# Performance work log

Hardware: AMD Instinct MI355X
Metric: run time of the kernel (lower is better)

The kernel has to match this reference:

```python
import jax, jax.numpy as jnp
import numpy as np

D_MODEL = 768
N_HEADS = 12
D_HEAD = 64
N_MEM = 3072
ALPHA = 0.1
EPS = 1e-5
W_SCALE = 0.02  # standard init scale so energies/grads stay well-conditioned


def setup_inputs() -> dict:
    key = jax.random.key(0)
    k0, k1, k2, k3 = jax.random.split(key, 4)
    B, S = 8, 1024
    x = jax.random.normal(k0, (B, S, D_MODEL), jnp.float32)
    gamma = jnp.ones((1,), jnp.float32)                      # scalar LN gamma (ET uses a single gamma)
    delta = jnp.zeros((D_MODEL,), jnp.float32)               # LN bias
    Wq = jax.random.normal(k1, (N_HEADS, D_HEAD, D_MODEL), jnp.float32) * W_SCALE
    Wk = jax.random.normal(k2, (N_HEADS, D_HEAD, D_MODEL), jnp.float32) * W_SCALE
    beta = jnp.ones((N_HEADS,), jnp.float32) / np.sqrt(D_HEAD)  # per-head beta init 1/sqrt(d_head)
    xi = jax.random.normal(k3, (N_MEM, D_MODEL), jnp.float32) * W_SCALE
    return {"x": x, "gamma": gamma, "delta": delta, "Wq": Wq, "Wk": Wk,
            "beta": beta, "xi": xi, "n_steps": 12}


def _total_energy(x, gamma, delta, Wq, Wk, beta, xi):
    # --- EnergyLayerNorm: g = dL/dx, E_ln = <x, g> - L ---
    mean = jnp.mean(x, axis=-1, keepdims=True)
    xm = x - mean
    var = jnp.mean(xm * xm, axis=-1, keepdims=True)
    std = jnp.sqrt(var + EPS)
    g = gamma * xm / std + delta                       # (B,S,D)
    L = jnp.sum(D_MODEL * gamma * std) + jnp.sum(delta * x)
    e_ln = jnp.sum(x * g) - L
    # --- EnergyAttention: E = -sum_{b,h,q} (1/beta_h) * logsumexp_k(beta_h * Q.K) ---
    q = jnp.einsum('bsd,hyd->bhsy', g, Wq)
    k = jnp.einsum('bsd,hyd->bhsy', g, Wk)
    A = jnp.einsum('bhqy,bhky->bhqk', q, k)            # (B,H,S,S)
    lse = jax.nn.logsumexp(beta[None, :, None, None] * A, axis=-1)  # (B,H,S)
    e_attn = -jnp.sum(lse / beta[None, :, None])
    # --- HopfieldNetwork: E = -1/2 sum relu(g @ xi^T)^2 ---
    h = jnp.einsum('bsd,md->bsm', g, xi)               # (B,S,M)
    e_hop = -0.5 * jnp.sum(jnp.square(jax.nn.relu(h)))
    return e_ln + e_attn + e_hop


def reference(x, gamma, delta, Wq, Wk, beta, xi, n_steps):
    grad_fn = jax.grad(_total_energy, argnums=0)

    def step(state, _):
        return state - ALPHA * grad_fn(state, gamma, delta, Wq, Wk, beta, xi), None

    final, _ = jax.lax.scan(step, x, None, length=n_steps)
    return final
```

## Files before the change

kernel.cpp:

```cpp
#include <hip/hip_runtime.h>
#include <hip/hip_bf16.h>
#include <stdint.h>

#define T_TOK 8192
#define DM    768
#define NH    12
#define DH    64
#define SEQ   1024
#define NBH   96
#define NMEM  3072
#define NUP   4608
#define ALPHA 0.1f
#define EPS   1e-5f
#define NSTEPS 12
#define PAD   72
#define SPLITK 4

typedef unsigned short us;
typedef __bf16 bf16x8 __attribute__((ext_vector_type(8)));
typedef float  f32x4  __attribute__((ext_vector_type(4)));

__device__ __forceinline__ us f2bf(float f) {
  uint32_t u = __builtin_bit_cast(uint32_t, f);
  u += 0x7fffu + ((u >> 16) & 1u);
  return (us)(u >> 16);
}

__device__ __forceinline__ f32x4 mfma16(bf16x8 a, bf16x8 b, f32x4 c) {
  return __builtin_amdgcn_mfma_f32_16x16x32_bf16(a, b, c, 0, 0, 0);
}

__device__ __forceinline__ void gld16(const void* g, void* l) {
  __builtin_amdgcn_global_load_lds(
      (const __attribute__((address_space(1))) void*)(uintptr_t)g,
      (__attribute__((address_space(3))) void*)(uint32_t)(uintptr_t)l,
      16, 0, 0);
}

__device__ __forceinline__ float block_sum(float v, float* sb, int tid) {
#pragma unroll
  for (int d = 32; d >= 1; d >>= 1) v += __shfl_xor(v, d);
  __syncthreads();
  if ((tid & 63) == 0) sb[tid >> 6] = v;
  __syncthreads();
  return sb[0] + sb[1] + sb[2] + sb[3];
}

__global__ __launch_bounds__(256) void pack_w(const float* __restrict__ Wq,
                                              const float* __restrict__ Wk,
                                              const float* __restrict__ xi,
                                              us* __restrict__ Wup, us* __restrict__ WdT) {
  int idx = blockIdx.x * 256 + threadIdx.x;
  if (idx >= NUP * DM) return;
  int r = idx / DM, d = idx - r * DM;
  float v = (r < 768) ? Wq[idx] : (r < 1536 ? Wk[idx - 768 * DM] : xi[idx - 1536 * DM]);
  us h = f2bf(v);
  Wup[idx] = h;
  WdT[(size_t)d * NUP + r] = h;
}

__global__ __launch_bounds__(256) void ln_fwd(const float* __restrict__ X,
                                              const float* __restrict__ gamma,
                                              const float* __restrict__ delta,
                                              us* __restrict__ g_bf,
                                              float* __restrict__ meanb, float* __restrict__ rstdb) {
  int t = blockIdx.x, tid = threadIdx.x;
  const float* x = X + (size_t)t * DM;
  __shared__ float sb[4];
  float v0 = x[tid], v1 = x[tid + 256], v2 = x[tid + 512];
  float mean = block_sum(v0 + v1 + v2, sb, tid) * (1.0f / DM);
  float d0 = v0 - mean, d1 = v1 - mean, d2 = v2 - mean;
  float var = block_sum(d0 * d0 + d1 * d1 + d2 * d2, sb, tid) * (1.0f / DM);
  float rstd = rsqrtf(var + EPS);
  float gm = gamma[0];
  us* go = g_bf + (size_t)t * DM;
  go[tid]       = f2bf(gm * d0 * rstd + delta[tid]);
  go[tid + 256] = f2bf(gm * d1 * rstd + delta[tid + 256]);
  go[tid + 512] = f2bf(gm * d2 * rstd + delta[tid + 512]);
  if (tid == 0) { meanb[t] = mean; rstdb[t] = rstd; }
}

template <int MODE>
__global__ __launch_bounds__(256, 4) void gemm_bt(const us* __restrict__ A, const us* __restrict__ B,
                                                  int Kstride, int kchunk, us* __restrict__ QKout,
                                                  us* __restrict__ Dout, float* __restrict__ Gout) {
  __shared__ us As[2 * 128 * 32];
  __shared__ us Bs[2 * 128 * 32];
  int tid = threadIdx.x;
  int w = tid >> 6, lane = tid & 63, lm = lane & 15, lq = lane >> 4;
  int wm = (w >> 1) * 64, wn = (w & 1) * 64;

  int m0 = blockIdx.x * 128, n0 = blockIdx.y * 128;
  int kbeg = blockIdx.z * kchunk;
  int NT = kchunk >> 5;

  int sr  = tid >> 2;
  int k8s = (tid & 3) ^ ((tid >> 3) & 3);
  const us* pa = A + (size_t)(m0 + sr) * Kstride + kbeg + k8s * 8;
  const us* pb = B + (size_t)(n0 + sr) * Kstride + kbeg + k8s * 8;
  const size_t hstep = (size_t)64 * Kstride;
  us* dA0 = &As[tid * 8];
  us* dB0 = &Bs[tid * 8];

  int kx = (lq ^ ((lm >> 1) & 3)) * 8;
  const us* Ar = As + (wm + lm) * 32 + kx;
  const us* Br = Bs + (wn + lm) * 32 + kx;

  f32x4 zero4 = {0.f, 0.f, 0.f, 0.f};
  f32x4 acc[4][4];
#pragma unroll
  for (int i = 0; i < 4; i++)
#pragma unroll
    for (int j = 0; j < 4; j++) acc[i][j] = zero4;

#define STAGE(S, T) { gld16(pa + (size_t)(T) * 32,         dA0 + (S) * 4096);        \
                      gld16(pa + (size_t)(T) * 32 + hstep, dA0 + (S) * 4096 + 2048); \
                      gld16(pb + (size_t)(T) * 32,         dB0 + (S) * 4096);        \
                      gld16(pb + (size_t)(T) * 32 + hstep, dB0 + (S) * 4096 + 2048); }

  STAGE(0, 0);
  asm volatile("s_waitcnt vmcnt(0)" ::: "memory");
  __builtin_amdgcn_s_barrier();

#define ITER(T, S) {                                                            \
    if ((T) + 1 < NT) STAGE((S) ^ 1, (T) + 1);                                  \
    bf16x8 af_[4], bf_[4];                                                      \
    _Pragma("unroll") for (int x = 0; x < 4; x++)                               \
      af_[x] = *(const bf16x8*)(Ar + (S) * 4096 + x * 512);                     \
    _Pragma("unroll") for (int x = 0; x < 4; x++)                               \
      bf_[x] = *(const bf16x8*)(Br + (S) * 4096 + x * 512);                     \
    _Pragma("unroll") for (int mt = 0; mt < 4; mt++)                            \
      _Pragma("unroll") for (int nt = 0; nt < 4; nt++)                          \
        acc[mt][nt] = mfma16(bf_[nt], af_[mt], acc[mt][nt]);       \
    if ((T) + 1 < NT) {                                                         \
      asm volatile("s_waitcnt lgkmcnt(0)" ::: "memory");                        \
      asm volatile("s_waitcnt vmcnt(0)" ::: "memory");                          \
      __builtin_amdgcn_s_barrier();                                             \
    }                                                                           \
  }

  for (int t = 0; t < NT; t += 2) {
    ITER(t,     0);
    ITER(t + 1, 1);
  }
#undef ITER
#undef STAGE

  int cb = wn + lq * 4;
  if (MODE == 0 && n0 < 1536) {
#pragma unroll
    for (int mt = 0; mt < 4; mt++) {
      us* rowp = QKout + (size_t)(m0 + wm + mt * 16 + lm) * 1536 + n0 + cb;
#pragma unroll
      for (int nt = 0; nt < 4; nt++) {
        f32x4 v = acc[mt][nt];
        uint2 p;
        p.x = (uint32_t)f2bf(v[0]) | ((uint32_t)f2bf(v[1]) << 16);
        p.y = (uint32_t)f2bf(v[2]) | ((uint32_t)f2bf(v[3]) << 16);
        *(uint2*)(rowp + nt * 16) = p;
      }
    }
  } else if (MODE == 0) {
#pragma unroll
    for (int mt = 0; mt < 4; mt++) {
      us* rowp = Dout + (size_t)(m0 + wm + mt * 16 + lm) * NUP + n0 + cb;
#pragma unroll
      for (int nt = 0; nt < 4; nt++) {
        f32x4 v = acc[mt][nt];
        uint2 p;
        p.x = (uint32_t)f2bf(fmaxf(v[0], 0.f)) | ((uint32_t)f2bf(fmaxf(v[1], 0.f)) << 16);
        p.y = (uint32_t)f2bf(fmaxf(v[2], 0.f)) | ((uint32_t)f2bf(fmaxf(v[3], 0.f)) << 16);
        *(uint2*)(rowp + nt * 16) = p;
      }
    }
  } else {
    float* Gz = Gout + (size_t)blockIdx.z * T_TOK * DM;
#pragma unroll
    for (int mt = 0; mt < 4; mt++) {
      float* rowp = Gz + (size_t)(m0 + wm + mt * 16 + lm) * DM + n0 + cb;
#pragma unroll
      for (int nt = 0; nt < 4; nt++)
        *(f32x4*)(rowp + nt * 16) = acc[mt][nt];
    }
  }
}

__global__ __launch_bounds__(256) void transpose_qk(const us* __restrict__ QK,
                                                    us* __restrict__ Qt, us* __restrict__ Kt) {
  int bh = blockIdx.x, kt = blockIdx.y, which = blockIdx.z;
  int b = bh / NH, h = bh - b * NH;
  int tid = threadIdx.x;
  __shared__ us tile[64][72];
  int c0 = h * 64 + (which ? 768 : 0);
  us* dst = (which ? Kt : Qt) + (size_t)bh * 64 * 1024;
#pragma unroll
  for (int r = 0; r < 2; r++) {
    int key = r * 32 + (tid >> 3); int yb = (tid & 7) * 8;
    *(bf16x8*)&tile[key][yb] =
        *(const bf16x8*)&QK[(size_t)(b * SEQ + kt * 64 + key) * 1536 + c0 + yb];
  }
  __syncthreads();
#pragma unroll
  for (int r = 0; r < 2; r++) {
    int lin = r * 256 + tid; int y = lin >> 3; int kb = (lin & 7) * 8;
    __align__(16) us tmp[8];
#pragma unroll
    for (int j = 0; j < 8; j++) tmp[j] = tile[kb + j][y];
    *(bf16x8*)&dst[(size_t)y * 1024 + kt * 64 + kb] = *(bf16x8*)tmp;
  }
}

__global__ __launch_bounds__(256) void attn_fwd(const us* __restrict__ QK, const us* __restrict__ Ktg,
                                                const float* __restrict__ beta,
                                                us* __restrict__ Dbuf, float* __restrict__ lse) {
  __shared__ us Qs[64 * PAD];
  __shared__ us Ks[64 * PAD];
  __shared__ us Kts[64 * PAD];
  __shared__ us Ps[4 * 16 * PAD];
  int bh = blockIdx.x, qt = blockIdx.y;
  int b = bh / NH, h = bh - b * NH;
  int tid = threadIdx.x, w = tid >> 6, lane = tid & 63, lm = lane & 15, lq = lane >> 4;
  float betah = beta[h];
#pragma unroll
  for (int r = 0; r < 2; r++) {
    int row = r * 32 + (tid >> 3); int yb = (tid & 7) * 8;
    *(bf16x8*)&Qs[row * PAD + yb] =
        *(const bf16x8*)&QK[(size_t)(b * SEQ + qt * 64 + row) * 1536 + h * 64 + yb];
  }
  __syncthreads();
  bf16x8 aq0 = *(const bf16x8*)&Qs[(w * 16 + lm) * PAD + lq * 8];
  bf16x8 aq1 = *(const bf16x8*)&Qs[(w * 16 + lm) * PAD + 32 + lq * 8];
  f32x4 zero = {0.f, 0.f, 0.f, 0.f};
  f32x4 O[4] = {zero, zero, zero, zero};
  float lacc[4] = {0.f, 0.f, 0.f, 0.f};
  us* pw = &Ps[w * 16 * PAD];

  for (int kc = 0; kc < SEQ; kc += 64) {
    __syncthreads();
#pragma unroll
    for (int r = 0; r < 2; r++) {
      int row = r * 32 + (tid >> 3); int yb = (tid & 7) * 8;
      *(bf16x8*)&Ks[row * PAD + yb] =
          *(const bf16x8*)&QK[(size_t)(b * SEQ + kc + row) * 1536 + 768 + h * 64 + yb];
      int lin = r * 256 + tid; int y = lin >> 3; int kb = (lin & 7) * 8;
      *(bf16x8*)&Kts[y * PAD + kb] =
          *(const bf16x8*)&Ktg[(size_t)(bh * 64 + y) * 1024 + kc + kb];
    }
    __syncthreads();
#pragma unroll
    for (int kk = 0; kk < 4; kk++) {
      f32x4 s = mfma16(aq0, *(const bf16x8*)&Ks[(kk * 16 + lm) * PAD + lq * 8], zero);
      s = mfma16(aq1, *(const bf16x8*)&Ks[(kk * 16 + lm) * PAD + 32 + lq * 8], s);
#pragma unroll
      for (int r = 0; r < 4; r++) {
        float p = __expf(betah * s[r]);
        lacc[r] += p;
        pw[(lq * 4 + r) * PAD + kk * 16 + lm] = f2bf(p);
      }
    }
    bf16x8 pa0 = *(const bf16x8*)&pw[lm * PAD + lq * 8];
    bf16x8 pa1 = *(const bf16x8*)&pw[lm * PAD + 32 + lq * 8];
#pragma unroll
    for (int nt = 0; nt < 4; nt++) {
      O[nt] = mfma16(pa0, *(const bf16x8*)&Kts[(nt * 16 + lm) * PAD + lq * 8], O[nt]);
      O[nt] = mfma16(pa1, *(const bf16x8*)&Kts[(nt * 16 + lm) * PAD + 32 + lq * 8], O[nt]);
    }
  }
  float l[4];
#pragma unroll
  for (int r = 0; r < 4; r++) {
    float v = lacc[r];
    v += __shfl_xor(v, 1); v += __shfl_xor(v, 2);
    v += __shfl_xor(v, 4); v += __shfl_xor(v, 8);
    l[r] = v;
  }
  float inv[4];
#pragma unroll
  for (int r = 0; r < 4; r++) inv[r] = 1.f / l[r];
#pragma unroll
  for (int nt = 0; nt < 4; nt++)
#pragma unroll
    for (int r = 0; r < 4; r++) {
      int q = qt * 64 + w * 16 + lq * 4 + r;
      Dbuf[(size_t)(b * SEQ + q) * NUP + h * 64 + nt * 16 + lm] = f2bf(O[nt][r] * inv[r]);
    }
  if (lm == 0) {
#pragma unroll
    for (int r = 0; r < 4; r++)
      lse[bh * SEQ + qt * 64 + w * 16 + lq * 4 + r] = __logf(l[r]);
  }
}

__global__ __launch_bounds__(256) void attn_bwd(const us* __restrict__ QK, const us* __restrict__ Qtg,
                                                const float* __restrict__ lse,
                                                const float* __restrict__ beta,
                                                us* __restrict__ Dbuf) {
  __shared__ us Ks2[64 * PAD];
  __shared__ us Qs2[64 * PAD];
  __shared__ us Qts[64 * PAD];
  __shared__ us Ps[4 * 16 * PAD];
  int bh = blockIdx.x, kt = blockIdx.y;
  int b = bh / NH, h = bh - b * NH;
  int tid = threadIdx.x, w = tid >> 6, lane = tid & 63, lm = lane & 15, lq = lane >> 4;
  float betah = beta[h];
#pragma unroll
  for (int r = 0; r < 2; r++) {
    int row = r * 32 + (tid >> 3); int yb = (tid & 7) * 8;
    *(bf16x8*)&Ks2[row * PAD + yb] =
        *(const bf16x8*)&QK[(size_t)(b * SEQ + kt * 64 + row) * 1536 + 768 + h * 64 + yb];
  }
  __syncthreads();
  bf16x8 ak0 = *(const bf16x8*)&Ks2[(w * 16 + lm) * PAD + lq * 8];
  bf16x8 ak1 = *(const bf16x8*)&Ks2[(w * 16 + lm) * PAD + 32 + lq * 8];
  f32x4 zero = {0.f, 0.f, 0.f, 0.f};
  f32x4 O[4] = {zero, zero, zero, zero};
  us* pw = &Ps[w * 16 * PAD];

  for (int qc = 0; qc < SEQ; qc += 64) {
    __syncthreads();
#pragma unroll
    for (int r = 0; r < 2; r++) {
      int row = r * 32 + (tid >> 3); int yb = (tid & 7) * 8;
      *(bf16x8*)&Qs2[row * PAD + yb] =
          *(const bf16x8*)&QK[(size_t)(b * SEQ + qc + row) * 1536 + h * 64 + yb];
      int lin = r * 256 + tid; int y = lin >> 3; int qb = (lin & 7) * 8;
      *(bf16x8*)&Qts[y * PAD + qb] =
          *(const bf16x8*)&Qtg[(size_t)(bh * 64 + y) * 1024 + qc + qb];
    }
    __syncthreads();
#pragma unroll
    for (int kk = 0; kk < 4; kk++) {
      f32x4 s = mfma16(ak0, *(const bf16x8*)&Qs2[(kk * 16 + lm) * PAD + lq * 8], zero);
      s = mfma16(ak1, *(const bf16x8*)&Qs2[(kk * 16 + lm) * PAD + 32 + lq * 8], s);
      float lv = lse[bh * SEQ + qc + kk * 16 + lm];
#pragma unroll
      for (int r = 0; r < 4; r++)
        pw[(lq * 4 + r) * PAD + kk * 16 + lm] = f2bf(__expf(betah * s[r] - lv));
    }
    bf16x8 pa0 = *(const bf16x8*)&pw[lm * PAD + lq * 8];
    bf16x8 pa1 = *(const bf16x8*)&pw[lm * PAD + 32 + lq * 8];
#pragma unroll
    for (int nt = 0; nt < 4; nt++) {
      O[nt] = mfma16(pa0, *(const bf16x8*)&Qts[(nt * 16 + lm) * PAD + lq * 8], O[nt]);
      O[nt] = mfma16(pa1, *(const bf16x8*)&Qts[(nt * 16 + lm) * PAD + 32 + lq * 8], O[nt]);
    }
  }
#pragma unroll
  for (int nt = 0; nt < 4; nt++)
#pragma unroll
    for (int r = 0; r < 4; r++) {
      int key = kt * 64 + w * 16 + lq * 4 + r;
      Dbuf[(size_t)(b * SEQ + key) * NUP + 768 + h * 64 + nt * 16 + lm] = f2bf(O[nt][r]);
    }
}

__global__ __launch_bounds__(256) void update_x(float* __restrict__ X, const float* __restrict__ G,
                                                float* __restrict__ meanb,
                                                float* __restrict__ rstdb,
                                                const float* __restrict__ gamma,
                                                const float* __restrict__ delta,
                                                us* __restrict__ g_bf) {
  int t = blockIdx.x, tid = threadIdx.x;
  __shared__ float sb[4];
  float mean = meanb[t], rstd = rstdb[t], gm = gamma[0];
  float* x = X + (size_t)t * DM;
  const float* g0 = G + (size_t)t * DM;
  const size_t GS = (size_t)T_TOK * DM;
  int i0 = tid, i1 = tid + 256, i2 = tid + 512;
  float x0 = x[i0], x1 = x[i1], x2 = x[i2];
  float gv0 = 0.f, gv1 = 0.f, gv2 = 0.f;
#pragma unroll
  for (int z = 0; z < SPLITK; z++) {
    gv0 += g0[i0 + z * GS];
    gv1 += g0[i1 + z * GS];
    gv2 += g0[i2 + z * GS];
  }
  float v0 = x0 - gv0, v1 = x1 - gv1, v2 = x2 - gv2;
  float n0 = (x0 - mean) * rstd, n1 = (x1 - mean) * rstd, n2 = (x2 - mean) * rstd;
  float s1 = block_sum(v0 + v1 + v2, sb, tid) * (1.0f / DM);
  float s2 = block_sum(v0 * n0 + v1 * n1 + v2 * n2, sb, tid) * (1.0f / DM);
  float c = ALPHA * gm * rstd;
  float y0 = x0 - c * (v0 - s1 - n0 * s2);
  float y1 = x1 - c * (v1 - s1 - n1 * s2);
  float y2 = x2 - c * (v2 - s1 - n2 * s2);
  x[i0] = y0; x[i1] = y1; x[i2] = y2;
  float mean2 = block_sum(y0 + y1 + y2, sb, tid) * (1.0f / DM);
  float d0 = y0 - mean2, d1 = y1 - mean2, d2 = y2 - mean2;
  float var2 = block_sum(d0 * d0 + d1 * d1 + d2 * d2, sb, tid) * (1.0f / DM);
  float rstd2 = rsqrtf(var2 + EPS);
  us* go = g_bf + (size_t)t * DM;
  go[i0] = f2bf(gm * d0 * rstd2 + delta[i0]);
  go[i1] = f2bf(gm * d1 * rstd2 + delta[i1]);
  go[i2] = f2bf(gm * d2 * rstd2 + delta[i2]);
  if (tid == 0) { meanb[t] = mean2; rstdb[t] = rstd2; }
}

extern "C" void kernel_launch(void* const* d_in, const int* in_sizes, int n_in,
                              void* d_out, int out_size, void* d_ws, size_t ws_size,
                              hipStream_t stream) {
  const float* x_in  = (const float*)d_in[0];
  const float* gamma = (const float*)d_in[1];
  const float* delta = (const float*)d_in[2];
  const float* Wq    = (const float*)d_in[3];
  const float* Wk    = (const float*)d_in[4];
  const float* beta  = (const float*)d_in[5];
  const float* xi    = (const float*)d_in[6];
  float* X = (float*)d_out;

  char* p = (char*)d_ws;
  auto carve = [&](size_t bytes) -> char* {
    char* q = p; p += (bytes + 255) & ~(size_t)255; return q;
  };
  us*    g_bf  = (us*)carve((size_t)T_TOK * DM * 2);
  float* meanb = (float*)carve((size_t)T_TOK * 4);
  float* rstdb = (float*)carve((size_t)T_TOK * 4);
  us*    QK    = (us*)carve((size_t)T_TOK * 1536 * 2);
  float* G     = (float*)carve((size_t)SPLITK * T_TOK * DM * 4);
  us*    Qt    = (us*)G;
  us*    Kt    = Qt + (size_t)NBH * 64 * 1024;
  float* lseb  = (float*)carve((size_t)NBH * SEQ * 4);
  us*    Dbuf  = (us*)carve((size_t)T_TOK * NUP * 2);
  us*    Wup   = (us*)carve((size_t)NUP * DM * 2);
  us*    WdT   = (us*)carve((size_t)DM * NUP * 2);

  hipMemcpyAsync(X, x_in, (size_t)T_TOK * DM * 4, hipMemcpyDeviceToDevice, stream);
  pack_w<<<(NUP * DM + 255) / 256, 256, 0, stream>>>(Wq, Wk, xi, Wup, WdT);
  ln_fwd<<<T_TOK, 256, 0, stream>>>(X, gamma, delta, g_bf, meanb, rstdb);

  for (int s = 0; s < NSTEPS; s++) {
    gemm_bt<0><<<dim3(64, 36, 1), 256, 0, stream>>>(g_bf, Wup, DM, DM, QK, Dbuf, nullptr);
    transpose_qk<<<dim3(NBH, 16, 2), 256, 0, stream>>>(QK, Qt, Kt);
    attn_fwd<<<dim3(NBH, 16), 256, 0, stream>>>(QK, Kt, beta, Dbuf, lseb);
    attn_bwd<<<dim3(NBH, 16), 256, 0, stream>>>(QK, Qt, lseb, beta, Dbuf);
    gemm_bt<1><<<dim3(64, 6, SPLITK), 256, 0, stream>>>(Dbuf, WdT, NUP, NUP / SPLITK,
                                                        nullptr, nullptr, G);
    update_x<<<T_TOK, 256, 0, stream>>>(X, G, meanb, rstdb, gamma, delta, g_bf);
  }
}
```

Before: 3.605 ms.

## Double-buffer attention K/Q tiles with async global-to-LDS loads and XOR swizzle

Both attention kernels now stage the next 64-key (or 64-query) tile into a second LDS buffer with direct global-to-LDS loads while the current tile is processed. The padded layout is replaced by an XOR-swizzled 64-wide layout to avoid bank conflicts. The goal is to hide global load latency behind the MFMA work and to drop one barrier per iteration. In exchange LDS use per block grows and the launch bounds now ask for 3 blocks per CU, which may limit registers.

```diff
diff --git a/kernel.cpp b/kernel.cpp
--- a/kernel.cpp
+++ b/kernel.cpp
@@ -210,12 +210,12 @@
   }
 }
 
-__global__ __launch_bounds__(256) void attn_fwd(const us* __restrict__ QK, const us* __restrict__ Ktg,
-                                                const float* __restrict__ beta,
-                                                us* __restrict__ Dbuf, float* __restrict__ lse) {
+__global__ __launch_bounds__(256, 3) void attn_fwd(const us* __restrict__ QK, const us* __restrict__ Ktg,
+                                                   const float* __restrict__ beta,
+                                                   us* __restrict__ Dbuf, float* __restrict__ lse) {
   __shared__ us Qs[64 * PAD];
-  __shared__ us Ks[64 * PAD];
-  __shared__ us Kts[64 * PAD];
+  __shared__ us Ks[2 * 64 * 64];
+  __shared__ us Kts[2 * 64 * 64];
   __shared__ us Ps[4 * 16 * PAD];
   int bh = blockIdx.x, qt = blockIdx.y;
   int b = bh / NH, h = bh - b * NH;
@@ -235,22 +235,35 @@
   float lacc[4] = {0.f, 0.f, 0.f, 0.f};
   us* pw = &Ps[w * 16 * PAD];
 
+  int r0_ = tid >> 3;
+  int g0_ = (tid & 7) ^ (r0_ & 7);
+  const us* srcK  = &QK[(size_t)(b * SEQ + r0_) * 1536 + 768 + h * 64 + g0_ * 8];
+  const us* srcK2 = srcK + (size_t)32 * 1536;
+  const us* srcT  = &Ktg[(size_t)(bh * 64 + r0_) * 1024 + g0_ * 8];
+  const us* srcT2 = srcT + (size_t)32 * 1024;
+  us* dK = &Ks[tid * 8];
+  us* dT = &Kts[tid * 8];
+#define STG_F(S, KC) { gld16(srcK  + (size_t)(KC) * 1536, dK + (S) * 4096);        \
+                       gld16(srcK2 + (size_t)(KC) * 1536, dK + (S) * 4096 + 2048); \
+                       gld16(srcT  + (KC),                dT + (S) * 4096);        \
+                       gld16(srcT2 + (KC),                dT + (S) * 4096 + 2048); }
+
+  STG_F(0, 0);
+  asm volatile("s_waitcnt vmcnt(0)" ::: "memory");
+  __builtin_amdgcn_s_barrier();
+
+  int sw1 = (lq ^ (lm & 7)) * 8;
+  int sw2 = ((lq + 4) ^ (lm & 7)) * 8;
+  int S = 0;
   for (int kc = 0; kc < SEQ; kc += 64) {
-    __syncthreads();
-#pragma unroll
-    for (int r = 0; r < 2; r++) {
-      int row = r * 32 + (tid >> 3); int yb = (tid & 7) * 8;
-      *(bf16x8*)&Ks[row * PAD + yb] =
-          *(const bf16x8*)&QK[(size_t)(b * SEQ + kc + row) * 1536 + 768 + h * 64 + yb];
-      int lin = r * 256 + tid; int y = lin >> 3; int kb = (lin & 7) * 8;
-      *(bf16x8*)&Kts[y * PAD + kb] =
-          *(const bf16x8*)&Ktg[(size_t)(bh * 64 + y) * 1024 + kc + kb];
-    }
-    __syncthreads();
+    if (kc + 64 < SEQ) STG_F(S ^ 1, kc + 64);
+    const us* KsS  = Ks  + S * 4096;
+    const us* KtsS = Kts + S * 4096;
 #pragma unroll
     for (int kk = 0; kk < 4; kk++) {
-      f32x4 s = mfma16(aq0, *(const bf16x8*)&Ks[(kk * 16 + lm) * PAD + lq * 8], zero);
-      s = mfma16(aq1, *(const bf16x8*)&Ks[(kk * 16 + lm) * PAD + 32 + lq * 8], s);
+      int rb = (kk * 16 + lm) * 64;
+      f32x4 s = mfma16(aq0, *(const bf16x8*)(KsS + rb + sw1), zero);
+      s = mfma16(aq1, *(const bf16x8*)(KsS + rb + sw2), s);
 #pragma unroll
       for (int r = 0; r < 4; r++) {
         float p = __expf(betah * s[r]);
@@ -262,10 +275,18 @@
     bf16x8 pa1 = *(const bf16x8*)&pw[lm * PAD + 32 + lq * 8];
 #pragma unroll
     for (int nt = 0; nt < 4; nt++) {
-      O[nt] = mfma16(pa0, *(const bf16x8*)&Kts[(nt * 16 + lm) * PAD + lq * 8], O[nt]);
-      O[nt] = mfma16(pa1, *(const bf16x8*)&Kts[(nt * 16 + lm) * PAD + 32 + lq * 8], O[nt]);
-    }
-  }
+      int rb = (nt * 16 + lm) * 64;
+      O[nt] = mfma16(pa0, *(const bf16x8*)(KtsS + rb + sw1), O[nt]);
+      O[nt] = mfma16(pa1, *(const bf16x8*)(KtsS + rb + sw2), O[nt]);
+    }
+    if (kc + 64 < SEQ) {
+      asm volatile("s_waitcnt lgkmcnt(0)" ::: "memory");
+      asm volatile("s_waitcnt vmcnt(0)" ::: "memory");
+      __builtin_amdgcn_s_barrier();
+    }
+    S ^= 1;
+  }
+#undef STG_F
   float l[4];
 #pragma unroll
   for (int r = 0; r < 4; r++) {
@@ -291,13 +312,13 @@
   }
 }
 
-__global__ __launch_bounds__(256) void attn_bwd(const us* __restrict__ QK, const us* __restrict__ Qtg,
-                                                const float* __restrict__ lse,
-                                                const float* __restrict__ beta,
-                                                us* __restrict__ Dbuf) {
+__global__ __launch_bounds__(256, 3) void attn_bwd(const us* __restrict__ QK, const us* __restrict__ Qtg,
+                                                   const float* __restrict__ lse,
+                                                   const float* __restrict__ beta,
+                                                   us* __restrict__ Dbuf) {
   __shared__ us Ks2[64 * PAD];
-  __shared__ us Qs2[64 * PAD];
-  __shared__ us Qts[64 * PAD];
+  __shared__ us Qs2[2 * 64 * 64];
+  __shared__ us Qts[2 * 64 * 64];
   __shared__ us Ps[4 * 16 * PAD];
   int bh = blockIdx.x, kt = blockIdx.y;
   int b = bh / NH, h = bh - b * NH;
@@ -316,22 +337,35 @@
   f32x4 O[4] = {zero, zero, zero, zero};
   us* pw = &Ps[w * 16 * PAD];
 
+  int r0_ = tid >> 3;
+  int g0_ = (tid & 7) ^ (r0_ & 7);
+  const us* srcQ  = &QK[(size_t)(b * SEQ + r0_) * 1536 + h * 64 + g0_ * 8];
+  const us* srcQ2 = srcQ + (size_t)32 * 1536;
+  const us* srcT  = &Qtg[(size_t)(bh * 64 + r0_) * 1024 + g0_ * 8];
+  const us* srcT2 = srcT + (size_t)32 * 1024;
+  us* dQ = &Qs2[tid * 8];
+  us* dT = &Qts[tid * 8];
+#define STG_B(S, QC) { gld16(srcQ  + (size_t)(QC) * 1536, dQ + (S) * 4096);        \
+                       gld16(srcQ2 + (size_t)(QC) * 1536, dQ + (S) * 4096 + 2048); \
+                       gld16(srcT  + (QC),                dT + (S) * 4096);        \
+                       gld16(srcT2 + (QC),                dT + (S) * 4096 + 2048); }
+
+  STG_B(0, 0);
+  asm volatile("s_waitcnt vmcnt(0)" ::: "memory");
+  __builtin_amdgcn_s_barrier();
+
+  int sw1 = (lq ^ (lm & 7)) * 8;
+  int sw2 = ((lq + 4) ^ (lm & 7)) * 8;
+  int S = 0;
   for (int qc = 0; qc < SEQ; qc += 64) {
-    __syncthreads();
-#pragma unroll
-    for (int r = 0; r < 2; r++) {
-      int row = r * 32 + (tid >> 3); int yb = (tid & 7) * 8;
-      *(bf16x8*)&Qs2[row * PAD + yb] =
-          *(const bf16x8*)&QK[(size_t)(b * SEQ + qc + row) * 1536 + h * 64 + yb];
-      int lin = r * 256 + tid; int y = lin >> 3; int qb = (lin & 7) * 8;
-      *(bf16x8*)&Qts[y * PAD + qb] =
-          *(const bf16x8*)&Qtg[(size_t)(bh * 64 + y) * 1024 + qc + qb];
-    }
-    __syncthreads();
+    if (qc + 64 < SEQ) STG_B(S ^ 1, qc + 64);
+    const us* QsS  = Qs2 + S * 4096;
+    const us* QtsS = Qts + S * 4096;
 #pragma unroll
     for (int kk = 0; kk < 4; kk++) {
-      f32x4 s = mfma16(ak0, *(const bf16x8*)&Qs2[(kk * 16 + lm) * PAD + lq * 8], zero);
-      s = mfma16(ak1, *(const bf16x8*)&Qs2[(kk * 16 + lm) * PAD + 32 + lq * 8], s);
+      int rb = (kk * 16 + lm) * 64;
+      f32x4 s = mfma16(ak0, *(const bf16x8*)(QsS + rb + sw1), zero);
+      s = mfma16(ak1, *(const bf16x8*)(QsS + rb + sw2), s);
       float lv = lse[bh * SEQ + qc + kk * 16 + lm];
 #pragma unroll
       for (int r = 0; r < 4; r++)
@@ -341,10 +375,18 @@
     bf16x8 pa1 = *(const bf16x8*)&pw[lm * PAD + 32 + lq * 8];
 #pragma unroll
     for (int nt = 0; nt < 4; nt++) {
-      O[nt] = mfma16(pa0, *(const bf16x8*)&Qts[(nt * 16 + lm) * PAD + lq * 8], O[nt]);
-      O[nt] = mfma16(pa1, *(const bf16x8*)&Qts[(nt * 16 + lm) * PAD + 32 + lq * 8], O[nt]);
-    }
-  }
+      int rb = (nt * 16 + lm) * 64;
+      O[nt] = mfma16(pa0, *(const bf16x8*)(QtsS + rb + sw1), O[nt]);
+      O[nt] = mfma16(pa1, *(const bf16x8*)(QtsS + rb + sw2), O[nt]);
+    }
+    if (qc + 64 < SEQ) {
+      asm volatile("s_waitcnt lgkmcnt(0)" ::: "memory");
+      asm volatile("s_waitcnt vmcnt(0)" ::: "memory");
+      __builtin_amdgcn_s_barrier();
+    }
+    S ^= 1;
+  }
+#undef STG_B
 #pragma unroll
   for (int nt = 0; nt < 4; nt++)
 #pragma unroll
```

Result: no change. 3.656 ms (+1.4%).

## Split gemm into dedicated up/down kernels with 256x256 tiles and triple buffering

Applied to the files above, without the earlier changes.

Splits the templated GEMM into a dedicated up-projection kernel and a new down-projection kernel. The down kernel uses 512 threads, 256x256 output tiles, a three-stage LDS pipeline and an XCD-aware block remapping. The goal is higher data reuse per block and better L2 locality across chiplets. The trade-off is far fewer blocks (384), which risks poor CU occupancy and a wave-quantization tail, plus higher LDS and register use.

```diff
diff --git a/kernel.cpp b/kernel.cpp
--- a/kernel.cpp
+++ b/kernel.cpp
@@ -80,25 +80,21 @@
   if (tid == 0) { meanb[t] = mean; rstdb[t] = rstd; }
 }
 
-template <int MODE>
-__global__ __launch_bounds__(256, 4) void gemm_bt(const us* __restrict__ A, const us* __restrict__ B,
-                                                  int Kstride, int kchunk, us* __restrict__ QKout,
-                                                  us* __restrict__ Dout, float* __restrict__ Gout) {
+__global__ __launch_bounds__(256, 4) void gemm_up(const us* __restrict__ A, const us* __restrict__ B,
+                                                  us* __restrict__ QKout, us* __restrict__ Dout) {
   __shared__ us As[2 * 128 * 32];
   __shared__ us Bs[2 * 128 * 32];
   int tid = threadIdx.x;
   int w = tid >> 6, lane = tid & 63, lm = lane & 15, lq = lane >> 4;
   int wm = (w >> 1) * 64, wn = (w & 1) * 64;
-
   int m0 = blockIdx.x * 128, n0 = blockIdx.y * 128;
-  int kbeg = blockIdx.z * kchunk;
-  int NT = kchunk >> 5;
+  const int NT = DM / 32;
 
   int sr  = tid >> 2;
   int k8s = (tid & 3) ^ ((tid >> 3) & 3);
-  const us* pa = A + (size_t)(m0 + sr) * Kstride + kbeg + k8s * 8;
-  const us* pb = B + (size_t)(n0 + sr) * Kstride + kbeg + k8s * 8;
-  const size_t hstep = (size_t)64 * Kstride;
+  const us* pa = A + (size_t)(m0 + sr) * DM + k8s * 8;
+  const us* pb = B + (size_t)(n0 + sr) * DM + k8s * 8;
+  const size_t hstep = (size_t)64 * DM;
   us* dA0 = &As[tid * 8];
   us* dB0 = &Bs[tid * 8];
 
@@ -147,7 +143,7 @@
 #undef STAGE
 
   int cb = wn + lq * 4;
-  if (MODE == 0 && n0 < 1536) {
+  if (n0 < 1536) {
 #pragma unroll
     for (int mt = 0; mt < 4; mt++) {
       us* rowp = QKout + (size_t)(m0 + wm + mt * 16 + lm) * 1536 + n0 + cb;
@@ -160,7 +156,7 @@
         *(uint2*)(rowp + nt * 16) = p;
       }
     }
-  } else if (MODE == 0) {
+  } else {
 #pragma unroll
     for (int mt = 0; mt < 4; mt++) {
       us* rowp = Dout + (size_t)(m0 + wm + mt * 16 + lm) * NUP + n0 + cb;
@@ -173,15 +169,92 @@
         *(uint2*)(rowp + nt * 16) = p;
       }
     }
-  } else {
-    float* Gz = Gout + (size_t)blockIdx.z * T_TOK * DM;
-#pragma unroll
-    for (int mt = 0; mt < 4; mt++) {
-      float* rowp = Gz + (size_t)(m0 + wm + mt * 16 + lm) * DM + n0 + cb;
-#pragma unroll
-      for (int nt = 0; nt < 4; nt++)
-        *(f32x4*)(rowp + nt * 16) = acc[mt][nt];
-    }
+  }
+}
+
+__global__ __launch_bounds__(512, 2) void gemm_dn(const us* __restrict__ A, const us* __restrict__ B,
+                                                  int kchunk, float* __restrict__ Gout) {
+  __shared__ us As[3 * 256 * 32];
+  __shared__ us Bs[3 * 256 * 32];
+  int tid = threadIdx.x;
+  int w = tid >> 6, lane = tid & 63, lm = lane & 15, lq = lane >> 4;
+  int wm = w >> 2, wn = w & 3;
+
+  int nwg  = gridDim.x * gridDim.y;
+  int id   = blockIdx.y * gridDim.x + blockIdx.x;
+  int qq   = nwg >> 3, rr = nwg & 7;
+  int xcd  = id & 7, rank = id >> 3;
+  int nid  = (xcd < rr ? xcd * (qq + 1) : rr * (qq + 1) + (xcd - rr) * qq) + rank;
+  int bm   = nid % gridDim.x, bn = nid / gridDim.x;
+  int m0 = bm * 256, n0 = bn * 256;
+  int kbeg = blockIdx.z * kchunk;
+  int NT = kchunk >> 5;
+
+  int sr  = w * 16 + (lane >> 2);
+  int k8s = (lane & 3) ^ ((lane >> 3) & 3);
+  const us* pa = A + (size_t)(m0 + sr) * NUP + kbeg + k8s * 8;
+  const us* pb = B + (size_t)(n0 + sr) * NUP + kbeg + k8s * 8;
+  const size_t hstep = (size_t)128 * NUP;
+  us* dA0 = &As[tid * 8];
+  us* dB0 = &Bs[tid * 8];
+
+  int kx   = (lq ^ ((lm >> 1) & 3)) * 8;
+  int aoff = (wm * 128 + lm) * 32 + kx;
+  int boff = (wn * 64  + lm) * 32 + kx;
+  const us* Ar = As + aoff;
+  const us* Br = Bs + boff;
+
+  f32x4 zero4 = {0.f, 0.f, 0.f, 0.f};
+  f32x4 acc[8][4];
+#pragma unroll
+  for (int i = 0; i < 8; i++)
+#pragma unroll
+    for (int j = 0; j < 4; j++) acc[i][j] = zero4;
+
+#define STAGE_A(S, T) { gld16(pa + (size_t)(T) * 32,         dA0 + (S) * 8192); \
+                        gld16(pa + (size_t)(T) * 32 + hstep, dA0 + (S) * 8192 + 4096); }
+#define STAGE_B(S, T) { gld16(pb + (size_t)(T) * 32,         dB0 + (S) * 8192); \
+                        gld16(pb + (size_t)(T) * 32 + hstep, dB0 + (S) * 8192 + 4096); }
+
+  STAGE_A(0, 0); STAGE_B(0, 0);
+  STAGE_A(1, 1); STAGE_B(1, 1);
+  asm volatile("s_waitcnt vmcnt(4)" ::: "memory");
+  __builtin_amdgcn_s_barrier();
+
+#define ITER(T, S) {                                                            \
+    bf16x8 af_[8], bf_[4];                                                      \
+    _Pragma("unroll") for (int x = 0; x < 8; x++)                               \
+      af_[x] = *(const bf16x8*)(Ar + (S) * 8192 + x * 512);                     \
+    _Pragma("unroll") for (int x = 0; x < 4; x++)                               \
+      bf_[x] = *(const bf16x8*)(Br + (S) * 8192 + x * 512);                     \
+    if ((T) + 2 < NT) { STAGE_A(((S) + 2) % 3, (T) + 2);                        \
+                        STAGE_B(((S) + 2) % 3, (T) + 2); }                      \
+    _Pragma("unroll") for (int mt = 0; mt < 8; mt++)                            \
+      _Pragma("unroll") for (int nt = 0; nt < 4; nt++)                          \
+        acc[mt][nt] = mfma16(bf_[nt], af_[mt], acc[mt][nt]);       \
+    asm volatile("s_waitcnt lgkmcnt(0)" ::: "memory");                          \
+    if ((T) + 2 < NT)      { asm volatile("s_waitcnt vmcnt(4)" ::: "memory"); } \
+    else if ((T) + 1 < NT) { asm volatile("s_waitcnt vmcnt(0)" ::: "memory"); } \
+    __builtin_amdgcn_s_barrier();                                               \
+  }
+
+  for (int t = 0; t < NT; t += 3) {
+    ITER(t,     0);
+    ITER(t + 1, 1);
+    ITER(t + 2, 2);
+  }
+#undef ITER
+#undef STAGE_A
+#undef STAGE_B
+
+  float* Gz = Gout + (size_t)blockIdx.z * T_TOK * DM;
+  int cb = wn * 64 + lq * 4;
+#pragma unroll
+  for (int mt = 0; mt < 8; mt++) {
+    float* rowp = Gz + (size_t)(m0 + wm * 128 + mt * 16 + lm) * DM + n0 + cb;
+#pragma unroll
+    for (int nt = 0; nt < 4; nt++)
+      *(f32x4*)(rowp + nt * 16) = acc[mt][nt];
   }
 }
 
@@ -428,12 +501,11 @@
   ln_fwd<<<T_TOK, 256, 0, stream>>>(X, gamma, delta, g_bf, meanb, rstdb);
 
   for (int s = 0; s < NSTEPS; s++) {
-    gemm_bt<0><<<dim3(64, 36, 1), 256, 0, stream>>>(g_bf, Wup, DM, DM, QK, Dbuf, nullptr);
+    gemm_up<<<dim3(64, 36), 256, 0, stream>>>(g_bf, Wup, QK, Dbuf);
     transpose_qk<<<dim3(NBH, 16, 2), 256, 0, stream>>>(QK, Qt, Kt);
     attn_fwd<<<dim3(NBH, 16), 256, 0, stream>>>(QK, Kt, beta, Dbuf, lseb);
     attn_bwd<<<dim3(NBH, 16), 256, 0, stream>>>(QK, Qt, lseb, beta, Dbuf);
-    gemm_bt<1><<<dim3(64, 6, SPLITK), 256, 0, stream>>>(Dbuf, WdT, NUP, NUP / SPLITK,
-                                                        nullptr, nullptr, G);
+    gemm_dn<<<dim3(32, 3, SPLITK), 512, 0, stream>>>(Dbuf, WdT, NUP / SPLITK, G);
     update_x<<<T_TOK, 256, 0, stream>>>(X, G, meanb, rstdb, gamma, delta, g_bf);
   }
 }
```

Result: no change. 3.669 ms (+1.8%).
